# Kernel optimization log

Hardware: AMD Instinct MI355X
Metric: run time of the kernel (lower is better)

## Reference

```python
import jax, jax.numpy as jnp
import numpy as np

BS, T, D_IN, D_H, D_OUT = 8, 4096, 1024, 1024, 1024


def setup_inputs() -> dict:
    key = jax.random.key(0)
    kx, ka, kb, kc = jax.random.split(key, 4)
    x = jax.random.normal(kx, (BS, T, D_IN), dtype=jnp.float32)
    # stable_init: uniform in [0.999, 1.001)
    a = jax.random.uniform(ka, (D_H,), minval=0.999, maxval=1.001, dtype=jnp.float32)
    # glorot_normal: std = sqrt(2 / (fan_in + fan_out))
    b = jax.random.normal(kb, (D_IN, D_H), dtype=jnp.float32) * np.sqrt(2.0 / (D_IN + D_H))
    c = jax.random.normal(kc, (D_H, D_OUT), dtype=jnp.float32) * np.sqrt(2.0 / (D_H + D_OUT))
    return {"x": x, "a": a, "b": b, "c": c}


def reference(x, a, b, c):
    # Precompute input projection as one big GEMM: u[b,t,h] = x @ b  (input-independent of recurrence)
    u = jnp.einsum('bti,ih->bth', x, b)
    u = jnp.swapaxes(u, 0, 1)  # [T, BS, H] for scan over time

    def step(h, u_t):
        h = h * a + u_t  # diagonal linear recurrence
        return h, h

    init = jnp.zeros((x.shape[0], a.shape[0]), dtype=x.dtype)
    _, hs = jax.lax.scan(step, init, u)  # hs: [T, BS, H]
    # Output projection as one batched GEMM, then back to [BS, T, D_OUT]
    y = jnp.einsum('tbh,ho->bto', hs, c)
    return y
```

## Files before the change

### kernel.cpp

```cpp
#include <hip/hip_runtime.h>
#include <hip/hip_bf16.h>
#include <stdint.h>

#define BS 8
#define TT 4096
#define DI 1024
#define DH 1024
#define DO 1024
#define M1 (BS*TT)
#define NC 64
#define CL (TT/NC)

typedef __attribute__((ext_vector_type(8))) __bf16 bf16x8;
typedef __attribute__((ext_vector_type(4))) __bf16 bf16x4;
typedef __attribute__((ext_vector_type(4))) float f32x4;

__global__ void conv_bf16_kernel(const float* __restrict__ in, __bf16* __restrict__ out, int n8) {
    int i = blockIdx.x * blockDim.x + threadIdx.x;
    int stride = gridDim.x * blockDim.x;
    for (; i < n8; i += stride) {
        f32x4 v0 = *(const f32x4*)&in[(size_t)i * 8];
        f32x4 v1 = *(const f32x4*)&in[(size_t)i * 8 + 4];
        bf16x8 o;
        o[0] = (__bf16)v0[0]; o[1] = (__bf16)v0[1]; o[2] = (__bf16)v0[2]; o[3] = (__bf16)v0[3];
        o[4] = (__bf16)v1[0]; o[5] = (__bf16)v1[1]; o[6] = (__bf16)v1[2]; o[7] = (__bf16)v1[3];
        *(bf16x8*)&out[(size_t)i * 8] = o;
    }
}

__global__ void transp_conv_kernel(const float* __restrict__ src, __bf16* __restrict__ dst,
                                   int K, int N) {
    __shared__ float tile[32][33];
    const int tx = threadIdx.x & 31;
    const int ty = threadIdx.x >> 5;
    const int k0 = blockIdx.x * 32;
    const int n0 = blockIdx.y * 32;
    #pragma unroll
    for (int i = 0; i < 32; i += 8)
        tile[ty + i][tx] = src[(size_t)(k0 + ty + i) * N + n0 + tx];
    __syncthreads();
    #pragma unroll
    for (int i = 0; i < 32; i += 8)
        dst[(size_t)(n0 + ty + i) * K + k0 + tx] = (__bf16)tile[tx][ty + i];
}

template<int OUTF32>
__global__ __launch_bounds__(256, 2) void gemm_bt_kernel(
    const __bf16* __restrict__ A, const __bf16* __restrict__ Bt,
    __bf16* __restrict__ Obf, float* __restrict__ Of,
    int M, int N, int K)
{
    __shared__ __bf16 As[128 * 64];
    __shared__ __bf16 Bs[128 * 64];

    const int tid = threadIdx.x;
    const int w = tid >> 6;
    const int l = tid & 63;
    const int rowBase = blockIdx.x * 128;
    const int colBase = blockIdx.y * 128;
    const int wm = w >> 1, wn = w & 1;
    const int lr = l & 15;
    const int lk = (l >> 4) * 8;

    f32x4 acc[4][4];
    #pragma unroll
    for (int i = 0; i < 4; i++)
        #pragma unroll
        for (int j = 0; j < 4; j++)
            acc[i][j] = (f32x4){0.f, 0.f, 0.f, 0.f};

    const __bf16* Ag = A  + (size_t)(rowBase + w * 8 + (l >> 3)) * K + (l & 7) * 8;
    const __bf16* Bg = Bt + (size_t)(colBase + w * 8 + (l >> 3)) * K + (l & 7) * 8;
    __bf16* Asw = As + w * 512;
    __bf16* Bsw = Bs + w * 512;

    for (int kt = 0; kt < K; kt += 64) {
        #pragma unroll
        for (int i = 0; i < 4; i++) {
            __builtin_amdgcn_global_load_lds(
                (const __attribute__((address_space(1))) void*)(Ag + (size_t)(i * 32) * K + kt),
                (__attribute__((address_space(3))) void*)(Asw + i * 2048), 16, 0, 0);
            __builtin_amdgcn_global_load_lds(
                (const __attribute__((address_space(1))) void*)(Bg + (size_t)(i * 32) * K + kt),
                (__attribute__((address_space(3))) void*)(Bsw + i * 2048), 16, 0, 0);
        }
        __syncthreads();
        #pragma unroll
        for (int kk = 0; kk < 64; kk += 32) {
            bf16x8 af[4], bfr[4];
            #pragma unroll
            for (int m = 0; m < 4; m++)
                af[m] = *(bf16x8*)&As[(wm * 64 + m * 16 + lr) * 64 + kk + lk];
            #pragma unroll
            for (int n = 0; n < 4; n++)
                bfr[n] = *(bf16x8*)&Bs[(wn * 64 + n * 16 + lr) * 64 + kk + lk];
            #pragma unroll
            for (int m = 0; m < 4; m++)
                #pragma unroll
                for (int n = 0; n < 4; n++)
                    acc[m][n] = __builtin_amdgcn_mfma_f32_16x16x32_bf16(af[m], bfr[n], acc[m][n], 0, 0, 0);
        }
        __syncthreads();
    }

    const int orow = rowBase + wm * 64 + (l >> 4) * 4;
    const int ocol = colBase + wn * 64 + lr;
    #pragma unroll
    for (int m = 0; m < 4; m++)
        #pragma unroll
        for (int n = 0; n < 4; n++)
            #pragma unroll
            for (int j = 0; j < 4; j++) {
                size_t idx = (size_t)(orow + m * 16 + j) * N + ocol + n * 16;
                if constexpr (OUTF32) Of[idx] = acc[m][n][j];
                else                  Obf[idx] = (__bf16)acc[m][n][j];
            }
}

__global__ void scan1_kernel(const __bf16* __restrict__ u, const float* __restrict__ a,
                             float* __restrict__ E) {
    int g = blockIdx.x * blockDim.x + threadIdx.x;
    int c4 = g & 255;
    int rest = g >> 8;
    int k = rest & (NC - 1);
    int b = rest >> 6;
    int ch = c4 * 4;
    f32x4 av = { a[ch], a[ch + 1], a[ch + 2], a[ch + 3] };
    size_t base = ((size_t)(b * TT + k * CL)) * DH + ch;
    f32x4 h = {0.f, 0.f, 0.f, 0.f};
    for (int t = 0; t < CL; t++) {
        bf16x4 v = *(const bf16x4*)&u[base + (size_t)t * DH];
        h[0] = h[0] * av[0] + (float)v[0];
        h[1] = h[1] * av[1] + (float)v[1];
        h[2] = h[2] * av[2] + (float)v[2];
        h[3] = h[3] * av[3] + (float)v[3];
    }
    *(f32x4*)&E[((size_t)(b * NC + k)) * DH + ch] = h;
}

__global__ void scan2_kernel(const float* __restrict__ E, const float* __restrict__ a,
                             float* __restrict__ Cc) {
    int g = blockIdx.x * blockDim.x + threadIdx.x;
    int ch = g & (DH - 1);
    int b = g >> 10;
    float av = a[ch];
    float aL = av;
    #pragma unroll
    for (int i = 0; i < 6; i++) aL *= aL;
    float carry = 0.f;
    for (int k = 0; k < NC; k++) {
        size_t idx = ((size_t)(b * NC + k)) * DH + ch;
        Cc[idx] = carry;
        carry = aL * carry + E[idx];
    }
}

__global__ void scan3_kernel(__bf16* __restrict__ u, const float* __restrict__ a,
                             const float* __restrict__ Cc) {
    int g = blockIdx.x * blockDim.x + threadIdx.x;
    int c4 = g & 255;
    int rest = g >> 8;
    int k = rest & (NC - 1);
    int b = rest >> 6;
    int ch = c4 * 4;
    f32x4 av = { a[ch], a[ch + 1], a[ch + 2], a[ch + 3] };
    f32x4 p = *(const f32x4*)&Cc[((size_t)(b * NC + k)) * DH + ch];
    f32x4 h = {0.f, 0.f, 0.f, 0.f};
    size_t base = ((size_t)(b * TT + k * CL)) * DH + ch;
    for (int t = 0; t < CL; t++) {
        size_t idx = base + (size_t)t * DH;
        bf16x4 v = *(bf16x4*)&u[idx];
        h[0] = h[0] * av[0] + (float)v[0];
        h[1] = h[1] * av[1] + (float)v[1];
        h[2] = h[2] * av[2] + (float)v[2];
        h[3] = h[3] * av[3] + (float)v[3];
        p[0] *= av[0]; p[1] *= av[1]; p[2] *= av[2]; p[3] *= av[3];
        bf16x4 o;
        o[0] = (__bf16)(h[0] + p[0]);
        o[1] = (__bf16)(h[1] + p[1]);
        o[2] = (__bf16)(h[2] + p[2]);
        o[3] = (__bf16)(h[3] + p[3]);
        *(bf16x4*)&u[idx] = o;
    }
}

extern "C" void kernel_launch(void* const* d_in, const int* in_sizes, int n_in,
                              void* d_out, int out_size, void* d_ws, size_t ws_size,
                              hipStream_t stream) {
    const float* x = (const float*)d_in[0];
    const float* a = (const float*)d_in[1];
    const float* b = (const float*)d_in[2];
    const float* c = (const float*)d_in[3];
    float* y = (float*)d_out;

    char* ws = (char*)d_ws;
    size_t off = 0;
    __bf16* u  = (__bf16*)(ws + off); off += (size_t)M1 * DH * 2;
    __bf16* bT = (__bf16*)(ws + off); off += (size_t)DI * DH * 2;
    __bf16* cT = (__bf16*)(ws + off); off += (size_t)DH * DO * 2;
    if (ws_size < off) return;

    __bf16* xbf = (__bf16*)d_out;
    float*  E   = (float*)((char*)d_out + (size_t)M1 * DI * 2);
    float*  Cc  = E + (size_t)BS * NC * DH;

    conv_bf16_kernel<<<2048, 256, 0, stream>>>(x, xbf, (M1 * DI) / 8);
    transp_conv_kernel<<<dim3(DI / 32, DH / 32), 256, 0, stream>>>(b, bT, DI, DH);
    transp_conv_kernel<<<dim3(DH / 32, DO / 32), 256, 0, stream>>>(c, cT, DH, DO);
    gemm_bt_kernel<0><<<dim3(M1 / 128, DH / 128), 256, 0, stream>>>(xbf, bT, u, nullptr, M1, DH, DI);
    scan1_kernel<<<(BS * NC * (DH / 4)) / 256, 256, 0, stream>>>(u, a, E);
    scan2_kernel<<<(BS * DH) / 256, 256, 0, stream>>>(E, a, Cc);
    scan3_kernel<<<(BS * NC * (DH / 4)) / 256, 256, 0, stream>>>(u, a, Cc);
    gemm_bt_kernel<1><<<dim3(M1 / 128, DO / 128), 256, 0, stream>>>(u, cT, nullptr, y, M1, DO, DH);
}
```

Measured before the change: 263.0 us.

## Replace GEMM with 256x256 tile, double-buffered LDS pipeline and swizzled layout

Swaps the 128x128 single-buffered bf16 GEMM for a 256x256-tile, 8-wave kernel that double-buffers 64-wide K slices in 128KB of LDS. It interleaves async global-to-LDS loads with MFMA phases using partial vmcnt waits and barriers. It also XOR-swizzles the LDS layout to avoid bank conflicts and raises wave priority around the MFMA bursts. The goal is to hide memory latency and raise arithmetic intensity, at the cost of heavy LDS use that limits occupancy and of fragile hand-written synchronisation.

Result: faster. 231.1 us (-12.1%).

```diff
diff --git a/kernel.cpp b/kernel.cpp
--- a/kernel.cpp
+++ b/kernel.cpp
@@ -45,76 +45,150 @@
 }
 
 template<int OUTF32>
-__global__ __launch_bounds__(256, 2) void gemm_bt_kernel(
+__global__ __launch_bounds__(512, 2) void gemm256_kernel(
     const __bf16* __restrict__ A, const __bf16* __restrict__ Bt,
     __bf16* __restrict__ Obf, float* __restrict__ Of,
     int M, int N, int K)
 {
-    __shared__ __bf16 As[128 * 64];
-    __shared__ __bf16 Bs[128 * 64];
-
+    __shared__ __bf16 lds[65536];
     const int tid = threadIdx.x;
-    const int w = tid >> 6;
-    const int l = tid & 63;
-    const int rowBase = blockIdx.x * 128;
-    const int colBase = blockIdx.y * 128;
-    const int wm = w >> 1, wn = w & 1;
+    const int wv = tid >> 6;
+    const int l  = tid & 63;
+    const int sr = wv >> 2;
+    const int sc = wv & 3;
     const int lr = l & 15;
     const int lk = (l >> 4) * 8;
-
-    f32x4 acc[4][4];
-    #pragma unroll
-    for (int i = 0; i < 4; i++)
+    const int xsw = (lr & 7) * 8;
+    const int ak0 = lk ^ xsw, ak1 = (32 + lk) ^ xsw;
+    const int rowBase = blockIdx.x * 256;
+    const int colBase = blockIdx.y * 256;
+    const int aOff = (sr * 64 + lr) * 64;
+    const int bOff = (sc * 32 + lr) * 64;
+    const int csw = ((l & 7) ^ (l >> 3)) * 8;
+    const __bf16* aSrc0 = A  + (size_t)(rowBase + wv * 16 + (l >> 3)) * K + csw;
+    const __bf16* bSrc0 = Bt + (size_t)(colBase + wv * 16 + (l >> 3)) * K + csw;
+
+    f32x4 acc[2][2][4][2];
+    #pragma unroll
+    for (int a0 = 0; a0 < 2; a0++)
         #pragma unroll
-        for (int j = 0; j < 4; j++)
-            acc[i][j] = (f32x4){0.f, 0.f, 0.f, 0.f};
-
-    const __bf16* Ag = A  + (size_t)(rowBase + w * 8 + (l >> 3)) * K + (l & 7) * 8;
-    const __bf16* Bg = Bt + (size_t)(colBase + w * 8 + (l >> 3)) * K + (l & 7) * 8;
-    __bf16* Asw = As + w * 512;
-    __bf16* Bsw = Bs + w * 512;
-
-    for (int kt = 0; kt < K; kt += 64) {
-        #pragma unroll
-        for (int i = 0; i < 4; i++) {
-            __builtin_amdgcn_global_load_lds(
-                (const __attribute__((address_space(1))) void*)(Ag + (size_t)(i * 32) * K + kt),
-                (__attribute__((address_space(3))) void*)(Asw + i * 2048), 16, 0, 0);
-            __builtin_amdgcn_global_load_lds(
-                (const __attribute__((address_space(1))) void*)(Bg + (size_t)(i * 32) * K + kt),
-                (__attribute__((address_space(3))) void*)(Bsw + i * 2048), 16, 0, 0);
-        }
-        __syncthreads();
-        #pragma unroll
-        for (int kk = 0; kk < 64; kk += 32) {
-            bf16x8 af[4], bfr[4];
-            #pragma unroll
-            for (int m = 0; m < 4; m++)
-                af[m] = *(bf16x8*)&As[(wm * 64 + m * 16 + lr) * 64 + kk + lk];
-            #pragma unroll
-            for (int n = 0; n < 4; n++)
-                bfr[n] = *(bf16x8*)&Bs[(wn * 64 + n * 16 + lr) * 64 + kk + lk];
+        for (int b0 = 0; b0 < 2; b0++)
             #pragma unroll
             for (int m = 0; m < 4; m++)
                 #pragma unroll
-                for (int n = 0; n < 4; n++)
-                    acc[m][n] = __builtin_amdgcn_mfma_f32_16x16x32_bf16(af[m], bfr[n], acc[m][n], 0, 0, 0);
-        }
-        __syncthreads();
-    }
-
-    const int orow = rowBase + wm * 64 + (l >> 4) * 4;
-    const int ocol = colBase + wn * 64 + lr;
-    #pragma unroll
-    for (int m = 0; m < 4; m++)
+                for (int n = 0; n < 2; n++)
+                    acc[a0][b0][m][n] = (f32x4){0.f, 0.f, 0.f, 0.f};
+
+    bf16x8 aF[4][2], bF[2][2];
+
+#define GLD(s, d) __builtin_amdgcn_global_load_lds( \
+        (const __attribute__((address_space(1))) void*)(s), \
+        (__attribute__((address_space(3))) void*)(d), 16, 0, 0)
+#define STAGE_A(buf, half, ktE) do { \
+        const __bf16* s_ = aSrc0 + (size_t)(half) * 128 * K + (ktE); \
+        __bf16* d_ = &lds[((buf) * 2 + (half)) * 8192 + wv * 1024]; \
+        GLD(s_, d_); GLD(s_ + (size_t)8 * K, d_ + 512); } while (0)
+#define STAGE_B(buf, half, ktE) do { \
+        const __bf16* s_ = bSrc0 + (size_t)(half) * 128 * K + (ktE); \
+        __bf16* d_ = &lds[32768 + ((buf) * 2 + (half)) * 8192 + wv * 1024]; \
+        GLD(s_, d_); GLD(s_ + (size_t)8 * K, d_ + 512); } while (0)
+#define LOADA(buf, qr) do { \
+        const __bf16* Ab_ = &lds[((buf) * 2 + (qr)) * 8192 + aOff]; \
+        _Pragma("unroll") \
+        for (int m = 0; m < 4; m++) { \
+            aF[m][0] = *(const bf16x8*)&Ab_[m * 1024 + ak0]; \
+            aF[m][1] = *(const bf16x8*)&Ab_[m * 1024 + ak1]; } } while (0)
+#define LOADB(buf, qc) do { \
+        const __bf16* Bb_ = &lds[32768 + ((buf) * 2 + (qc)) * 8192 + bOff]; \
+        _Pragma("unroll") \
+        for (int n = 0; n < 2; n++) { \
+            bF[n][0] = *(const bf16x8*)&Bb_[n * 1024 + ak0]; \
+            bF[n][1] = *(const bf16x8*)&Bb_[n * 1024 + ak1]; } } while (0)
+#define MM(qr, qc) do { \
+        __builtin_amdgcn_s_setprio(1); \
+        _Pragma("unroll") \
+        for (int m = 0; m < 4; m++) \
+            _Pragma("unroll") \
+            for (int n = 0; n < 2; n++) { \
+                acc[qr][qc][m][n] = __builtin_amdgcn_mfma_f32_16x16x32_bf16(aF[m][0], bF[n][0], acc[qr][qc][m][n], 0, 0, 0); \
+                acc[qr][qc][m][n] = __builtin_amdgcn_mfma_f32_16x16x32_bf16(aF[m][1], bF[n][1], acc[qr][qc][m][n], 0, 0, 0); } \
+        __builtin_amdgcn_s_setprio(0); } while (0)
+#define PHEND() do { __builtin_amdgcn_sched_barrier(0); __builtin_amdgcn_s_barrier(); } while (0)
+#define PHEND_W(cond) do { __builtin_amdgcn_sched_barrier(0); \
+        if (cond) { asm volatile("s_waitcnt vmcnt(0)" ::: "memory"); } \
+        else      { asm volatile("s_waitcnt vmcnt(4)" ::: "memory"); } \
+        __builtin_amdgcn_s_barrier(); } while (0)
+
+    const int NIT = K >> 7;
+
+    STAGE_A(0, 0, 0); STAGE_A(0, 1, 0); STAGE_B(0, 0, 0); STAGE_B(0, 1, 0);
+    STAGE_A(1, 0, 64); STAGE_A(1, 1, 64); STAGE_B(1, 0, 64); STAGE_B(1, 1, 64);
+    asm volatile("s_waitcnt vmcnt(8)" ::: "memory");
+    __builtin_amdgcn_s_barrier();
+
+    for (int it = 0; it < NIT; ++it) {
+        const int ktOdd  = (2 * it + 1) * 64;
+        const int ktEv2  = (2 * it + 2) * 64;
+        const int ktOdd2 = (2 * it + 3) * 64;
+        const bool last = (it == NIT - 1);
+        LOADA(0, 0); LOADB(0, 0);
+        if (it > 0) STAGE_A(1, 1, ktOdd);
+        __builtin_amdgcn_s_barrier();
+        MM(0, 0); PHEND();
+        LOADA(0, 1);
+        if (it > 0) STAGE_B(1, 1, ktOdd);
+        __builtin_amdgcn_s_barrier();
+        MM(1, 0); PHEND();
+        LOADA(0, 0); LOADB(0, 1);
+        if (!last) STAGE_B(0, 0, ktEv2);
+        __builtin_amdgcn_s_barrier();
+        MM(0, 1); PHEND();
+        LOADA(0, 1);
+        if (!last) STAGE_A(0, 0, ktEv2);
+        __builtin_amdgcn_s_barrier();
+        MM(1, 1); PHEND_W(last);
+        LOADA(1, 0); LOADB(1, 0);
+        if (!last) STAGE_A(0, 1, ktEv2);
+        __builtin_amdgcn_s_barrier();
+        MM(0, 0); PHEND();
+        LOADA(1, 1);
+        if (!last) STAGE_B(0, 1, ktEv2);
+        __builtin_amdgcn_s_barrier();
+        MM(1, 0); PHEND();
+        LOADA(1, 0); LOADB(1, 1);
+        if (!last) STAGE_B(1, 0, ktOdd2);
+        __builtin_amdgcn_s_barrier();
+        MM(0, 1); PHEND();
+        LOADA(1, 1);
+        if (!last) STAGE_A(1, 0, ktOdd2);
+        __builtin_amdgcn_s_barrier();
+        MM(1, 1); PHEND_W(last);
+    }
+
+    #pragma unroll
+    for (int qr = 0; qr < 2; qr++)
         #pragma unroll
-        for (int n = 0; n < 4; n++)
+        for (int qc = 0; qc < 2; qc++)
             #pragma unroll
-            for (int j = 0; j < 4; j++) {
-                size_t idx = (size_t)(orow + m * 16 + j) * N + ocol + n * 16;
-                if constexpr (OUTF32) Of[idx] = acc[m][n][j];
-                else                  Obf[idx] = (__bf16)acc[m][n][j];
-            }
+            for (int m = 0; m < 4; m++)
+                #pragma unroll
+                for (int n = 0; n < 2; n++)
+                    #pragma unroll
+                    for (int j = 0; j < 4; j++) {
+                        int row = rowBase + qr * 128 + sr * 64 + m * 16 + (l >> 4) * 4 + j;
+                        int col = colBase + qc * 128 + sc * 32 + n * 16 + lr;
+                        size_t idx = (size_t)row * N + col;
+                        if constexpr (OUTF32) Of[idx] = acc[qr][qc][m][n][j];
+                        else                  Obf[idx] = (__bf16)acc[qr][qc][m][n][j];
+                    }
+#undef GLD
+#undef STAGE_A
+#undef STAGE_B
+#undef LOADA
+#undef LOADB
+#undef MM
+#undef PHEND
+#undef PHEND_W
 }
 
 __global__ void scan1_kernel(const __bf16* __restrict__ u, const float* __restrict__ a,
@@ -207,9 +281,9 @@
     conv_bf16_kernel<<<2048, 256, 0, stream>>>(x, xbf, (M1 * DI) / 8);
     transp_conv_kernel<<<dim3(DI / 32, DH / 32), 256, 0, stream>>>(b, bT, DI, DH);
     transp_conv_kernel<<<dim3(DH / 32, DO / 32), 256, 0, stream>>>(c, cT, DH, DO);
-    gemm_bt_kernel<0><<<dim3(M1 / 128, DH / 128), 256, 0, stream>>>(xbf, bT, u, nullptr, M1, DH, DI);
+    gemm256_kernel<0><<<dim3(M1 / 256, DH / 256), 512, 0, stream>>>(xbf, bT, u, nullptr, M1, DH, DI);
     scan1_kernel<<<(BS * NC * (DH / 4)) / 256, 256, 0, stream>>>(u, a, E);
     scan2_kernel<<<(BS * DH) / 256, 256, 0, stream>>>(E, a, Cc);
     scan3_kernel<<<(BS * NC * (DH / 4)) / 256, 256, 0, stream>>>(u, a, Cc);
-    gemm_bt_kernel<1><<<dim3(M1 / 128, DO / 128), 256, 0, stream>>>(u, cT, nullptr, y, M1, DO, DH);
-}
+    gemm256_kernel<1><<<dim3(M1 / 256, DO / 256), 512, 0, stream>>>(u, cT, nullptr, y, M1, DO, DH);
+}
```
